# Kernel optimization log

Hardware: AMD Instinct MI355X
Metric: run time of the kernel (lower is better)

The kernel has to match this reference:

```python
import jax, jax.numpy as jnp
import numpy as np

GRID_RES = 128
K_PATHS = 8
SIGMA = 0.8
OFFSETS = jnp.array([[0,0,0],[0,0,1],[0,1,0],[0,1,1],[1,0,0],[1,0,1],[1,1,0],[1,1,1]], dtype=jnp.int32)


def setup_inputs() -> dict:
    key = jax.random.key(0)
    ks = jax.random.split(key, 8)
    N = 500000
    M = 500000
    x_source_ref = jax.random.uniform(ks[0], (N, 3), jnp.float32)
    x_source_curr = jnp.clip(x_source_ref + 0.02 * jax.random.normal(ks[1], (N, 3), jnp.float32), 0.0, 1.0)
    x_query_ref = jax.random.uniform(ks[2], (M, 3), jnp.float32)
    def dense(k, fan_in, fan_out):
        return (jax.random.normal(k, (fan_in, fan_out), jnp.float32) / np.sqrt(fan_in)).astype(jnp.float32)
    return {
        'x_query_ref': x_query_ref,
        'x_source_ref': x_source_ref,
        'x_source_curr': x_source_curr,
        'W_f': dense(ks[3], 3, 3), 'b_f': jnp.zeros((3,), jnp.float32),
        'W_d1': dense(ks[4], 24, 64), 'b_d1': jnp.zeros((64,), jnp.float32),
        'W_d2': dense(ks[5], 64, 64), 'b_d2': jnp.zeros((64,), jnp.float32),
        'W_d3': dense(ks[6], 64, 3), 'b_d3': jnp.zeros((3,), jnp.float32),
    }


def _p2g(content, coords):
    # 8-corner trilinear scatter-add: content [N,C] at float coords [N,3] -> flat grid [R^3, C]
    R = GRID_RES
    base = jnp.floor(coords).astype(jnp.int32)            # [N,3]
    d = coords - base.astype(coords.dtype)                # [N,3] fractional part
    off = OFFSETS[:, None, :]                             # [8,1,3]
    w = jnp.prod(jnp.where(off == 1, d[None], 1.0 - d[None]), axis=-1)  # [8,N]
    idx = base[None] + off                                # [8,N,3]
    flat = (idx[..., 0] * R + idx[..., 1]) * R + idx[..., 2]            # [8,N]
    C = content.shape[-1]
    vals = content[None] * w[..., None]                   # [8,N,C]
    return jnp.zeros((R ** 3, C), content.dtype).at[flat.reshape(-1)].add(vals.reshape(-1, C))


def _trilerp(flat_grid, pts):
    # order-1 map_coordinates, mode='nearest': weights from unclipped coords, indices clipped
    R = GRID_RES
    lo = jnp.floor(pts).astype(jnp.int32)                 # [P,3]
    fr = pts - lo.astype(pts.dtype)
    i0 = jnp.clip(lo, 0, R - 1)
    i1 = jnp.clip(lo + 1, 0, R - 1)
    out = jnp.zeros((pts.shape[0], flat_grid.shape[-1]), flat_grid.dtype)
    for c in range(8):  # fixed 8 corners, keeps peak memory at one [P,C] gather at a time
        ox, oy, oz = OFFSETS[c, 0], OFFSETS[c, 1], OFFSETS[c, 2]
        ix = jnp.where(ox == 1, i1[:, 0], i0[:, 0])
        iy = jnp.where(oy == 1, i1[:, 1], i0[:, 1])
        iz = jnp.where(oz == 1, i1[:, 2], i0[:, 2])
        wx = jnp.where(ox == 1, fr[:, 0], 1.0 - fr[:, 0])
        wy = jnp.where(oy == 1, fr[:, 1], 1.0 - fr[:, 1])
        wz = jnp.where(oz == 1, fr[:, 2], 1.0 - fr[:, 2])
        flat = (ix * R + iy) * R + iz
        out = out + flat_grid[flat] * (wx * wy * wz)[:, None]
    return out


def _posenc(x, L=3):
    outs = []
    for i in range(L):
        freq = (2.0 ** i) * jnp.pi
        outs.append(jnp.sin(freq * x))
        outs.append(jnp.cos(freq * x))
    return jnp.concatenate(outs, axis=-1)


def _forward(x_query_ref, x_source_ref, x_source_curr, W_f, b_f, W_d1, b_d1, W_d2, b_d2, W_d3, b_d3):
    R = GRID_RES
    xs = jnp.clip(x_source_ref, 0.0, 1.0)
    xq = jnp.clip(x_query_ref, 0.0, 1.0)
    u = x_source_curr - xs
    f_trans = jax.nn.gelu(u @ W_f + b_f)
    content = jnp.concatenate([f_trans, jnp.ones((u.shape[0], 1), u.dtype), u], axis=-1)  # [N,7]
    coords = jnp.clip(xs * (R - 1), 0.0, R - 1.001)
    flat_grid = _p2g(content, coords)                     # [R^3, 7]
    q = xq * (R - 1)                                      # [M,3]
    M = q.shape[0]
    noise = jax.random.normal(jax.random.key(42), (K_PATHS, M, 3), q.dtype) * SIGMA
    pts = (q[None] + noise).reshape(-1, 3)                # [K*M,3]
    samples = _trilerp(flat_grid, pts).reshape(K_PATHS, M, -1)
    raw = jnp.mean(samples, axis=0)                       # [M,7]
    grid_f, grid_d, grid_u = raw[:, :3], raw[:, 3:4], raw[:, 4:7]
    denom = jnp.maximum(grid_d, 1e-5)
    mask = (grid_d > 1e-5).astype(raw.dtype)
    f_norm = grid_f / denom * mask
    u_norm = grid_u / denom * mask
    dec = jnp.concatenate([f_norm, u_norm, _posenc(xq)], axis=-1)  # [M,24]
    h = jax.nn.gelu(dec @ W_d1 + b_d1)
    h = jax.nn.gelu(h @ W_d2 + b_d2)
    res = h @ W_d3 + b_d3
    return jnp.clip(u_norm + res, 0.001, 0.999)


def reference(x_query_ref, x_source_ref, x_source_curr, W_f, b_f, W_d1, b_d1, W_d2, b_d2, W_d3, b_d3):
    return _forward(x_query_ref, x_source_ref, x_source_curr, W_f, b_f, W_d1, b_d1, W_d2, b_d2, W_d3, b_d3)
```

## Files before the change

kernel.cpp:

```cpp
#include <hip/hip_runtime.h>
#include <cstdint>

#ifndef JAX_PARTITIONABLE
#define JAX_PARTITIONABLE 1
#endif

#define NCELLS (128*128*128)
#define SCAN_BLOCKS 1024
#define NQBINS (32*32*32)

typedef _Float16 f16;
typedef f16  half8 __attribute__((ext_vector_type(8)));
typedef f16  half4 __attribute__((ext_vector_type(4)));
typedef float f32x4 __attribute__((ext_vector_type(4)));

#define WSTR 40
#define DSTR 40
#define W2STR 72

#define GRID_SCALE 1024.0f
#define GRID_ISCALE 0.0009765625f

__device__ __forceinline__ uint32_t rotl32(uint32_t v, int s){ return (v << s) | (v >> (32 - s)); }

__device__ __forceinline__ void tf2x32(uint32_t& x0, uint32_t& x1){
  const uint32_t k0 = 0u, k1 = 42u;
  const uint32_t k2 = 0x1BD11BDAu ^ k0 ^ k1;
  x0 += k0; x1 += k1;
#define TFR(r) { x0 += x1; x1 = rotl32(x1,(r)); x1 ^= x0; }
  TFR(13) TFR(15) TFR(26) TFR(6)
  x0 += k1; x1 += k2 + 1u;
  TFR(17) TFR(29) TFR(16) TFR(24)
  x0 += k2; x1 += k0 + 2u;
  TFR(13) TFR(15) TFR(26) TFR(6)
  x0 += k0; x1 += k1 + 3u;
  TFR(17) TFR(29) TFR(16) TFR(24)
  x0 += k1; x1 += k2 + 4u;
  TFR(13) TFR(15) TFR(26) TFR(6)
  x0 += k2; x1 += k0 + 5u;
#undef TFR
}

__device__ __forceinline__ float erfinv_xla(float x){
  float w = -log1pf(-x*x);
  float p;
  if (w < 5.0f){
    w -= 2.5f;
    p =  2.81022636e-08f;
    p = fmaf(p,w, 3.43273939e-07f);
    p = fmaf(p,w,-3.5233877e-06f);
    p = fmaf(p,w,-4.39150654e-06f);
    p = fmaf(p,w, 0.00021858087f);
    p = fmaf(p,w,-0.00125372503f);
    p = fmaf(p,w,-0.00417768164f);
    p = fmaf(p,w, 0.246640727f);
    p = fmaf(p,w, 1.50140941f);
  } else {
    w = sqrtf(w) - 3.0f;
    p = -0.000200214257f;
    p = fmaf(p,w, 0.000100950558f);
    p = fmaf(p,w, 0.00134934322f);
    p = fmaf(p,w,-0.00367342844f);
    p = fmaf(p,w, 0.00573950773f);
    p = fmaf(p,w,-0.0076224613f);
    p = fmaf(p,w, 0.00943887047f);
    p = fmaf(p,w, 1.00167406f);
    p = fmaf(p,w, 2.83297682f);
  }
  return p*x;
}

__device__ __forceinline__ float noise_at(uint32_t idx, uint32_t half){
#if JAX_PARTITIONABLE
  (void)half;
  uint32_t x0 = 0u, x1 = idx;
  tf2x32(x0, x1);
  uint32_t bits = x0 ^ x1;
#else
  uint32_t j  = (idx < half) ? idx : (idx - half);
  uint32_t x0 = j, x1 = j + half;
  tf2x32(x0, x1);
  uint32_t bits = (idx < half) ? x0 : x1;
#endif
  float f = __uint_as_float((bits >> 9) | 0x3f800000u) - 1.0f;
  float u = fmaxf(-0.99999994f, fmaf(f, 2.0f, -0.99999994f));
  return (1.41421356f * erfinv_xla(u)) * 0.8f;
}

__device__ __forceinline__ float gelu_f(float x){
  float t = x*x;
  float inner = x * fmaf(0.035677408136f, t, 0.7978845608028654f);
  float e = __expf(2.0f * inner);
  float r = __builtin_amdgcn_rcpf(e + 1.0f);
  return x - x*r;
}

__device__ __forceinline__ uint32_t pack2h(float a, float b){
  union { f16 h[2]; uint32_t u; } c;
  c.h[0] = (f16)(a * GRID_SCALE);
  c.h[1] = (f16)(b * GRID_SCALE);
  return c.u;
}

__device__ __forceinline__ void particle_cell(const float* xsr, int i,
                                              float& sx, float& sy, float& sz,
                                              int& bx, int& by, int& bz,
                                              float& dx, float& dy, float& dz){
  sx = fminf(fmaxf(xsr[3*i+0], 0.0f), 1.0f);
  sy = fminf(fmaxf(xsr[3*i+1], 0.0f), 1.0f);
  sz = fminf(fmaxf(xsr[3*i+2], 0.0f), 1.0f);
  float cx = fminf(fmaxf(sx*127.0f, 0.0f), 126.999f);
  float cy = fminf(fmaxf(sy*127.0f, 0.0f), 126.999f);
  float cz = fminf(fmaxf(sz*127.0f, 0.0f), 126.999f);
  float bxf = floorf(cx), byf = floorf(cy), bzf = floorf(cz);
  bx = (int)bxf; by = (int)byf; bz = (int)bzf;
  dx = cx - bxf; dy = cy - byf; dz = cz - bzf;
}

__device__ __forceinline__ int qbin_of(float qx01, float qy01, float qz01){
  int bx = min((int)(qx01*127.0f), 127) >> 2;
  int by = min((int)(qy01*127.0f), 127) >> 2;
  int bz = min((int)(qz01*127.0f), 127) >> 2;
  return (((bx<<5)+by)<<5)+bz;
}

__global__ void __launch_bounds__(256) hist2_kernel(
    const float* __restrict__ xsr, const float* __restrict__ xq,
    int* __restrict__ cnt, int* __restrict__ qcnt, int N, int M){
  int i = blockIdx.x*256 + threadIdx.x;
  if (i < N){
    float sx,sy,sz,dx,dy,dz; int bx,by,bz;
    particle_cell(xsr,i,sx,sy,sz,bx,by,bz,dx,dy,dz);
    atomicAdd(&cnt[(((bx<<7)+by)<<7)+bz], 1);
  }
  if (i < M){
    float qx01 = fminf(fmaxf(xq[3*i+0], 0.0f), 1.0f);
    float qy01 = fminf(fmaxf(xq[3*i+1], 0.0f), 1.0f);
    float qz01 = fminf(fmaxf(xq[3*i+2], 0.0f), 1.0f);
    atomicAdd(&qcnt[qbin_of(qx01,qy01,qz01)], 1);
  }
}

__global__ void __launch_bounds__(256) scan1_kernel(const int* __restrict__ cnt,
                                                    int* __restrict__ offs,
                                                    int* __restrict__ bsum){
  __shared__ int lds[256];
  int t = threadIdx.x;
  int base = blockIdx.x*2048 + t*8;
  const int4* c4 = reinterpret_cast<const int4*>(cnt + base);
  int4 a0 = c4[0], a1 = c4[1];
  int s = a0.x+a0.y+a0.z+a0.w + a1.x+a1.y+a1.z+a1.w;
  lds[t] = s; __syncthreads();
  for (int off = 1; off < 256; off <<= 1){
    int v = (t >= off) ? lds[t-off] : 0;
    __syncthreads();
    lds[t] += v;
    __syncthreads();
  }
  int run = lds[t] - s;
  if (t == 255) bsum[blockIdx.x] = lds[255];
  int* o = offs + base;
  o[0]=run; run+=a0.x; o[1]=run; run+=a0.y; o[2]=run; run+=a0.z; o[3]=run; run+=a0.w;
  o[4]=run; run+=a1.x; o[5]=run; run+=a1.y; o[6]=run; run+=a1.z; o[7]=run;
}

__global__ void __launch_bounds__(1024) scan2q_kernel(int* __restrict__ bsum,
                                                      const int* __restrict__ qcnt,
                                                      int* __restrict__ qcur){
  __shared__ int lds[1024];
  int t = threadIdx.x;
  int v = bsum[t];
  lds[t] = v; __syncthreads();
  for (int off = 1; off < 1024; off <<= 1){
    int u = (t >= off) ? lds[t-off] : 0;
    __syncthreads();
    lds[t] += u;
    __syncthreads();
  }
  bsum[t] = lds[t] - v;
  if (t == 1023) bsum[1024] = lds[1023];
  __syncthreads();
  int base = t*32;
  int loc[32];
  int s = 0;
#pragma unroll
  for (int j = 0; j < 32; ++j){ loc[j] = qcnt[base+j]; s += loc[j]; }
  lds[t] = s; __syncthreads();
  for (int off = 1; off < 1024; off <<= 1){
    int u = (t >= off) ? lds[t-off] : 0;
    __syncthreads();
    lds[t] += u;
    __syncthreads();
  }
  int run = lds[t] - s;
#pragma unroll
  for (int j = 0; j < 32; ++j){ qcur[base+j] = run; run += loc[j]; }
}

__global__ void __launch_bounds__(256) scan3_kernel(int* __restrict__ offs,
                                                    const int* __restrict__ bsum,
                                                    int* __restrict__ cursor){
  int i = blockIdx.x*256 + threadIdx.x;
  int o = offs[i] + bsum[i >> 11];
  offs[i] = o; cursor[i] = o;
  if (i == 0) offs[NCELLS] = bsum[SCAN_BLOCKS];
}

__global__ void __launch_bounds__(256) scatter2_kernel(
    const float* __restrict__ xsr, const float* __restrict__ xsc,
    const float* __restrict__ Wf,  const float* __restrict__ bf,
    const float* __restrict__ xq,
    int* __restrict__ cursor, int* __restrict__ qcur,
    float4* __restrict__ pf, float4* __restrict__ pu, float* __restrict__ pz,
    float* __restrict__ qs, int* __restrict__ qidx, int N, int M){
  int i = blockIdx.x*256 + threadIdx.x;
  if (i < N){
    float sx,sy,sz,dx,dy,dz; int bx,by,bz;
    particle_cell(xsr,i,sx,sy,sz,bx,by,bz,dx,dy,dz);
    float ux = xsc[3*i+0] - sx;
    float uy = xsc[3*i+1] - sy;
    float uz = xsc[3*i+2] - sz;
    float f0 = gelu_f(ux*Wf[0] + uy*Wf[3] + uz*Wf[6] + bf[0]);
    float f1 = gelu_f(ux*Wf[1] + uy*Wf[4] + uz*Wf[7] + bf[1]);
    float f2 = gelu_f(ux*Wf[2] + uy*Wf[5] + uz*Wf[8] + bf[2]);
    int bin = (((bx<<7)+by)<<7)+bz;
    int pos = atomicAdd(&cursor[bin], 1);
    pf[pos] = make_float4(f0, f1, f2, dx);
    pu[pos] = make_float4(ux, uy, uz, dy);
    pz[pos] = dz;
  }
  if (i < M){
    float qx01 = fminf(fmaxf(xq[3*i+0], 0.0f), 1.0f);
    float qy01 = fminf(fmaxf(xq[3*i+1], 0.0f), 1.0f);
    float qz01 = fminf(fmaxf(xq[3*i+2], 0.0f), 1.0f);
    int pos = atomicAdd(&qcur[qbin_of(qx01,qy01,qz01)], 1);
    qs[3*pos+0] = qx01; qs[3*pos+1] = qy01; qs[3*pos+2] = qz01;
    qidx[pos] = i;
  }
}

__global__ void __launch_bounds__(256) p2g_gather_pair_kernel(
    const int* __restrict__ offs,
    const float4* __restrict__ pf, const float4* __restrict__ pu,
    const float* __restrict__ pz, uint4* __restrict__ gridh){
  int tid = blockIdx.x*256 + threadIdx.x;
  int zg = tid & 63, y = (tid >> 6) & 127, x = tid >> 13;
  int z0 = zg << 1;
  float a0[2]={0,0},a1[2]={0,0},a2[2]={0,0},a3[2]={0,0},a4[2]={0,0},a5[2]={0,0},a6[2]={0,0};
#pragma unroll
  for (int ox = 0; ox < 2; ++ox){
    int bx = x - ox; if (bx < 0) continue;
#pragma unroll
    for (int oy = 0; oy < 2; ++oy){
      int by = y - oy; if (by < 0) continue;
      int b0 = ((((bx<<7)+by)<<7)) + z0;
      int em = offs[b0];
      int sm = (z0 > 0) ? offs[b0-1] : em;
      int e0 = offs[b0+1];
      int e1 = offs[b0+2];
      for (int p = sm; p < e1; ++p){
        float4 A = pf[p]; float4 B = pu[p]; float dz = pz[p];
        float wx = ox ? A.w : 1.0f - A.w;
        float wy = oy ? B.w : 1.0f - B.w;
        float wxy = wx*wy;
        float omdz = 1.0f - dz;
        float w0 = (p < em) ? dz : ((p < e0) ? omdz : 0.0f);
        float w1 = (p < em) ? 0.0f : ((p < e0) ? dz : omdz);
        w0 *= wxy; w1 *= wxy;
        a0[0]=fmaf(A.x,w0,a0[0]); a1[0]=fmaf(A.y,w0,a1[0]); a2[0]=fmaf(A.z,w0,a2[0]);
        a3[0]+=w0; a4[0]=fmaf(B.x,w0,a4[0]); a5[0]=fmaf(B.y,w0,a5[0]); a6[0]=fmaf(B.z,w0,a6[0]);
        a0[1]=fmaf(A.x,w1,a0[1]); a1[1]=fmaf(A.y,w1,a1[1]); a2[1]=fmaf(A.z,w1,a2[1]);
        a3[1]+=w1; a4[1]=fmaf(B.x,w1,a4[1]); a5[1]=fmaf(B.y,w1,a5[1]); a6[1]=fmaf(B.z,w1,a6[1]);
      }
    }
  }
  int cell0 = ((((x<<7)+y)<<7)) + z0;
  uint4 g0, g1;
  g0.x = pack2h(a0[0], a1[0]); g0.y = pack2h(a2[0], a4[0]);
  g0.z = pack2h(a5[0], a6[0]); g0.w = __float_as_uint(a3[0]);
  g1.x = pack2h(a0[1], a1[1]); g1.y = pack2h(a2[1], a4[1]);
  g1.z = pack2h(a5[1], a6[1]); g1.w = __float_as_uint(a3[1]);
  uint4* g = gridh + cell0;
  g[0] = g0; g[1] = g1;
}

__global__ void __launch_bounds__(256, 4) gather_mlp_sorted_kernel(
    const float* __restrict__ qs,  const int* __restrict__ qidx,
    const uint4* __restrict__ gridh,
    const float* __restrict__ W1,  const float* __restrict__ b1,
    const float* __restrict__ W2,  const float* __restrict__ b2,
    const float* __restrict__ W3,  const float* __restrict__ b3,
    float* __restrict__ out, int M, int nblk)
{
  __shared__ __align__(16) f16  decs[4][64*DSTR];
  __shared__ __align__(16) f16  w1t[64*WSTR];
  __shared__ __align__(16) f16  w2t[64*W2STR];
  __shared__ __align__(16) float b1s[64], b2s[64];
  __shared__ __align__(16) float w3s[64*4];

  for (int i = threadIdx.x; i < 64*32; i += 256){
    int n = i >> 5, k = i & 31;
    w1t[n*WSTR + k] = (k < 24) ? (f16)W1[k*64 + n] : (f16)0.0f;
  }
  for (int i = threadIdx.x; i < 64*64; i += 256){
    int n = i >> 6, k = i & 63;
    w2t[n*W2STR + k] = (f16)W2[k*64 + n];
  }
  if (threadIdx.x < 64){ b1s[threadIdx.x] = b1[threadIdx.x]; b2s[threadIdx.x] = b2[threadIdx.x]; }
  for (int i = threadIdx.x; i < 192; i += 256){
    w3s[(i/3)*4 + (i - (i/3)*3)] = W3[i];
  }
  __syncthreads();

  int b = blockIdx.x;
  int nb8 = (nblk >> 3) << 3;
  int c = (b < nb8) ? ((b & 7)*(nblk >> 3) + (b >> 3)) : b;
  int t = c*256 + (int)threadIdx.x;
  bool active = (t < M);
  int tc = active ? t : (M - 1);
  int m = qidx[tc];

  float qx01 = qs[3*tc+0], qy01 = qs[3*tc+1], qz01 = qs[3*tc+2];
  float qx = qx01*127.0f, qy = qy01*127.0f, qz = qz01*127.0f;

  float r0=0.f,r1=0.f,r2=0.f,r3=0.f,r4=0.f,r5=0.f,r6=0.f;
  const uint32_t KSTRIDE = 3u*(uint32_t)M;
  const uint32_t HALF    = 4u*KSTRIDE;
  uint32_t m3 = 3u*(uint32_t)m;

  for (int k = 0; k < 8; ++k) {
    uint32_t base = (uint32_t)k*KSTRIDE + m3;
    float px = qx + noise_at(base+0u, HALF);
    float py = qy + noise_at(base+1u, HALF);
    float pz = qz + noise_at(base+2u, HALF);
    float fxf = floorf(px), fyf = floorf(py), fzf = floorf(pz);
    float fx = px - fxf, fy = py - fyf, fz = pz - fzf;
    int lx = (int)fxf, ly = (int)fyf, lz = (int)fzf;
    int x0i = min(max(lx,0),127),   x1i = min(max(lx+1,0),127);
    int y0i = min(max(ly,0),127),   y1i = min(max(ly+1,0),127);
    int z0i = min(max(lz,0),127),   z1i = min(max(lz+1,0),127);
    float ex = 1.0f-fx, ey = 1.0f-fy, ez = 1.0f-fz;

    auto corner = [&](int xi,int yi,int zi,float w){
      uint4 q4 = gridh[(((xi<<7)+yi)<<7)+zi];
      union { uint32_t u; f16 h[2]; } c0, c1, c2;
      c0.u = q4.x; c1.u = q4.y; c2.u = q4.z;
      r0 = fmaf((float)c0.h[0], w, r0);
      r1 = fmaf((float)c0.h[1], w, r1);
      r2 = fmaf((float)c1.h[0], w, r2);
      r4 = fmaf((float)c1.h[1], w, r4);
      r5 = fmaf((float)c2.h[0], w, r5);
      r6 = fmaf((float)c2.h[1], w, r6);
      r3 = fmaf(__uint_as_float(q4.w), w, r3);
    };
    corner(x0i,y0i,z0i, ex*ey*ez);
    corner(x0i,y0i,z1i, ex*ey*fz);
    corner(x0i,y1i,z0i, ex*fy*ez);
    corner(x0i,y1i,z1i, ex*fy*fz);
    corner(x1i,y0i,z0i, fx*ey*ez);
    corner(x1i,y0i,z1i, fx*ey*fz);
    corner(x1i,y1i,z0i, fx*fy*ez);
    corner(x1i,y1i,z1i, fx*fy*fz);
  }

  float dmean = r3*0.125f;
  float denom = fmaxf(dmean, 1e-5f);
  float maskf = (dmean > 1e-5f) ? 1.0f : 0.0f;
  float s   = 0.125f/denom*maskf;
  float sfu = s * GRID_ISCALE;
  float un0 = r4*sfu, un1 = r5*sfu, un2 = r6*sfu;

  float dec[24];
  dec[0]=r0*sfu; dec[1]=r1*sfu; dec[2]=r2*sfu; dec[3]=un0; dec[4]=un1; dec[5]=un2;
  dec[6]  = __builtin_amdgcn_sinf(0.5f*qx01);
  dec[7]  = __builtin_amdgcn_sinf(0.5f*qy01);
  dec[8]  = __builtin_amdgcn_sinf(0.5f*qz01);
  dec[9]  = __builtin_amdgcn_cosf(0.5f*qx01);
  dec[10] = __builtin_amdgcn_cosf(0.5f*qy01);
  dec[11] = __builtin_amdgcn_cosf(0.5f*qz01);
  dec[12] = __builtin_amdgcn_sinf(qx01);
  dec[13] = __builtin_amdgcn_sinf(qy01);
  dec[14] = __builtin_amdgcn_sinf(qz01);
  dec[15] = __builtin_amdgcn_cosf(qx01);
  dec[16] = __builtin_amdgcn_cosf(qy01);
  dec[17] = __builtin_amdgcn_cosf(qz01);
  dec[18] = __builtin_amdgcn_sinf(2.0f*qx01);
  dec[19] = __builtin_amdgcn_sinf(2.0f*qy01);
  dec[20] = __builtin_amdgcn_sinf(2.0f*qz01);
  dec[21] = __builtin_amdgcn_cosf(2.0f*qx01);
  dec[22] = __builtin_amdgcn_cosf(2.0f*qy01);
  dec[23] = __builtin_amdgcn_cosf(2.0f*qz01);

  int lane = threadIdx.x & 63;
  int wv   = threadIdx.x >> 6;
  f16* hb = &decs[wv][0];
  int lo = lane & 15;
  int hi = lane >> 4;

  {
    half8 dh;
#pragma unroll
    for (int c4 = 0; c4 < 3; ++c4){
#pragma unroll
      for (int j = 0; j < 8; ++j) dh[j] = (f16)dec[c4*8 + j];
      *reinterpret_cast<half8*>(&hb[lane*DSTR + c4*8]) = dh;
    }
#pragma unroll
    for (int j = 0; j < 8; ++j) dh[j] = (f16)0.0f;
    *reinterpret_cast<half8*>(&hb[lane*DSTR + 24]) = dh;
  }

  half4 w1f[4][2];
#pragma unroll
  for (int a = 0; a < 4; ++a)
#pragma unroll
    for (int kb = 0; kb < 2; ++kb)
      w1f[a][kb] = *reinterpret_cast<const half4*>(&w1t[(16*a + lo)*WSTR + 16*kb + 4*hi]);

  half4 dff[4][2];
#pragma unroll
  for (int bq = 0; bq < 4; ++bq)
#pragma unroll
    for (int kb = 0; kb < 2; ++kb)
      dff[bq][kb] = *reinterpret_cast<const half4*>(&hb[(16*bq + lo)*DSTR + 16*kb + 4*hi]);

  half4 hv[4][4];
#pragma unroll
  for (int a = 0; a < 4; ++a){
    f32x4 zb = *reinterpret_cast<const f32x4*>(&b1s[16*a + 4*hi]);
#pragma unroll
    for (int bq = 0; bq < 4; ++bq){
      f32x4 z = __builtin_amdgcn_mfma_f32_16x16x16f16(w1f[a][0], dff[bq][0], zb, 0, 0, 0);
      z       = __builtin_amdgcn_mfma_f32_16x16x16f16(w1f[a][1], dff[bq][1], z,  0, 0, 0);
      half4 hvv;
#pragma unroll
      for (int p = 0; p < 4; ++p) hvv[p] = (f16)gelu_f(z[p]);
      hv[a][bq] = hvv;
    }
  }

  float part[4][3];
#pragma unroll
  for (int bq = 0; bq < 4; ++bq){ part[bq][0]=0.f; part[bq][1]=0.f; part[bq][2]=0.f; }

#pragma unroll
  for (int a2 = 0; a2 < 4; ++a2){
    half4 w2f[4];
#pragma unroll
    for (int kb = 0; kb < 4; ++kb)
      w2f[kb] = *reinterpret_cast<const half4*>(&w2t[(16*a2 + lo)*W2STR + 16*kb + 4*hi]);
    f32x4 zb2 = *reinterpret_cast<const f32x4*>(&b2s[16*a2 + 4*hi]);
#pragma unroll
    for (int bq = 0; bq < 4; ++bq){
      f32x4 z = __builtin_amdgcn_mfma_f32_16x16x16f16(w2f[0], hv[0][bq], zb2, 0, 0, 0);
      z       = __builtin_amdgcn_mfma_f32_16x16x16f16(w2f[1], hv[1][bq], z,   0, 0, 0);
      z       = __builtin_amdgcn_mfma_f32_16x16x16f16(w2f[2], hv[2][bq], z,   0, 0, 0);
      z       = __builtin_amdgcn_mfma_f32_16x16x16f16(w2f[3], hv[3][bq], z,   0, 0, 0);
#pragma unroll
      for (int p = 0; p < 4; ++p){
        f32x4 w3v = *reinterpret_cast<const f32x4*>(&w3s[(16*a2 + 4*hi + p)*4]);
        float g = gelu_f(z[p]);
        part[bq][0] = fmaf(g, w3v[0], part[bq][0]);
        part[bq][1] = fmaf(g, w3v[1], part[bq][1]);
        part[bq][2] = fmaf(g, w3v[2], part[bq][2]);
      }
    }
  }

#pragma unroll
  for (int bq = 0; bq < 4; ++bq)
#pragma unroll
    for (int cc = 0; cc < 3; ++cc){
      float v = part[bq][cc];
      v += __shfl_xor(v, 16, 64);
      v += __shfl_xor(v, 32, 64);
      part[bq][cc] = v;
    }

  float o0 = (hi==0) ? part[0][0] : (hi==1) ? part[1][0] : (hi==2) ? part[2][0] : part[3][0];
  float o1 = (hi==0) ? part[0][1] : (hi==1) ? part[1][1] : (hi==2) ? part[2][1] : part[3][1];
  float o2 = (hi==0) ? part[0][2] : (hi==1) ? part[1][2] : (hi==2) ? part[2][2] : part[3][2];
  o0 += b3[0]; o1 += b3[1]; o2 += b3[2];

  if (active){
    out[3*m+0] = fminf(fmaxf(un0 + o0, 0.001f), 0.999f);
    out[3*m+1] = fminf(fmaxf(un1 + o1, 0.001f), 0.999f);
    out[3*m+2] = fminf(fmaxf(un2 + o2, 0.001f), 0.999f);
  }
}

__global__ void __launch_bounds__(256) p2g_atomic_kernel(
    const float* __restrict__ xsr, const float* __restrict__ xsc,
    const float* __restrict__ Wf,  const float* __restrict__ bf,
    float* __restrict__ grid, int N)
{
  int i = blockIdx.x*256 + threadIdx.x;
  if (i >= N) return;
  float sx,sy,sz,dx,dy,dz; int bx,by,bz;
  particle_cell(xsr,i,sx,sy,sz,bx,by,bz,dx,dy,dz);
  float ux = xsc[3*i+0] - sx;
  float uy = xsc[3*i+1] - sy;
  float uz = xsc[3*i+2] - sz;
  float f0 = gelu_f(ux*Wf[0] + uy*Wf[3] + uz*Wf[6] + bf[0]);
  float f1 = gelu_f(ux*Wf[1] + uy*Wf[4] + uz*Wf[7] + bf[1]);
  float f2 = gelu_f(ux*Wf[2] + uy*Wf[5] + uz*Wf[8] + bf[2]);
  float ex = 1.0f - dx, ey = 1.0f - dy, ez = 1.0f - dz;
  auto splat = [&](int xi, int yi, int zi, float w){
    float* p = grid + ((size_t)((((xi<<7)+yi)<<7)+zi) << 3);
    unsafeAtomicAdd(p+0, f0*w);
    unsafeAtomicAdd(p+1, f1*w);
    unsafeAtomicAdd(p+2, f2*w);
    unsafeAtomicAdd(p+3, w);
    unsafeAtomicAdd(p+4, ux*w);
    unsafeAtomicAdd(p+5, uy*w);
    unsafeAtomicAdd(p+6, uz*w);
  };
  splat(bx,  by,  bz,   ex*ey*ez);
  splat(bx,  by,  bz+1, ex*ey*dz);
  splat(bx,  by+1,bz,   ex*dy*ez);
  splat(bx,  by+1,bz+1, ex*dy*dz);
  splat(bx+1,by,  bz,   dx*ey*ez);
  splat(bx+1,by,  bz+1, dx*ey*dz);
  splat(bx+1,by+1,bz,   dx*dy*ez);
  splat(bx+1,by+1,bz+1, dx*dy*dz);
}

__global__ void __launch_bounds__(256) grid2half_kernel(
    const float* __restrict__ grid, uint4* __restrict__ gridh){
  int i = blockIdx.x*256 + threadIdx.x;
  const float4* p = reinterpret_cast<const float4*>(grid + ((size_t)i << 3));
  float4 A = p[0], B = p[1];
  uint4 g;
  g.x = pack2h(A.x, A.y);
  g.y = pack2h(A.z, B.x);
  g.z = pack2h(B.y, B.z);
  g.w = __float_as_uint(A.w);
  gridh[i] = g;
}

__global__ void __launch_bounds__(256) qident_kernel(
    const float* __restrict__ xq, float* __restrict__ qs, int* __restrict__ qidx, int M){
  int i = blockIdx.x*256 + threadIdx.x;
  if (i >= M) return;
  qs[3*i+0] = fminf(fmaxf(xq[3*i+0], 0.0f), 1.0f);
  qs[3*i+1] = fminf(fmaxf(xq[3*i+1], 0.0f), 1.0f);
  qs[3*i+2] = fminf(fmaxf(xq[3*i+2], 0.0f), 1.0f);
  qidx[i] = i;
}

extern "C" void kernel_launch(void* const* d_in, const int* in_sizes, int n_in,
                              void* d_out, int out_size, void* d_ws, size_t ws_size,
                              hipStream_t stream)
{
  const float* xq  = (const float*)d_in[0];
  const float* xsr = (const float*)d_in[1];
  const float* xsc = (const float*)d_in[2];
  const float* Wf  = (const float*)d_in[3];
  const float* bf  = (const float*)d_in[4];
  const float* W1  = (const float*)d_in[5];
  const float* b1  = (const float*)d_in[6];
  const float* W2  = (const float*)d_in[7];
  const float* b2  = (const float*)d_in[8];
  const float* W3  = (const float*)d_in[9];
  const float* b3  = (const float*)d_in[10];
  float* out  = (float*)d_out;
  int M = in_sizes[0]/3;
  int N = in_sizes[1]/3;

  char* W = (char*)d_ws;
  size_t off = 0;
  auto alloc = [&](size_t bytes){ size_t o = off; off = (off + bytes + 255) & ~(size_t)255; return o; };
  size_t o_grid   = alloc((size_t)NCELLS * 8 * sizeof(float));
  size_t o_cnt    = alloc((size_t)NCELLS * sizeof(int));
  size_t o_qcnt   = alloc((size_t)NQBINS * sizeof(int));
  size_t o_offs   = alloc(((size_t)NCELLS + 1) * sizeof(int));
  size_t o_cursor = alloc((size_t)NCELLS * sizeof(int));
  size_t o_bsum   = alloc((size_t)(SCAN_BLOCKS + 1) * sizeof(int));
  size_t o_qcur   = alloc((size_t)NQBINS * sizeof(int));
  size_t o_pf     = alloc((size_t)N * sizeof(float4));
  size_t o_pu     = alloc((size_t)N * sizeof(float4));
  size_t o_pz     = alloc((size_t)N * sizeof(float));
  size_t o_qs     = alloc((size_t)M * 3 * sizeof(float));
  size_t o_qidx   = alloc((size_t)M * sizeof(int));
  size_t full_end = off;

  float*  grid   = (float*)(W + o_grid);
  int*    cnt    = (int*)(W + o_cnt);
  int*    qcnt   = (int*)(W + o_qcnt);
  int*    offs   = (int*)(W + o_offs);
  int*    cursor = (int*)(W + o_cursor);
  int*    bsum   = (int*)(W + o_bsum);
  int*    qcur   = (int*)(W + o_qcur);
  float4* pf     = (float4*)(W + o_pf);
  float4* pu     = (float4*)(W + o_pu);
  float*  pz     = (float*)(W + o_pz);
  float*  qs     = (float*)(W + o_qs);
  int*    qidx   = (int*)(W + o_qidx);

  int nthr = (N > M) ? N : M;
  int nblkNM = (nthr + 255) / 256;
  uint4* gridh;

  if (full_end <= ws_size) {
    gridh = (uint4*)(W + o_grid);
    hipMemsetAsync(cnt, 0, (size_t)NCELLS * sizeof(int) + (size_t)NQBINS * sizeof(int), stream);
    hist2_kernel<<<nblkNM, 256, 0, stream>>>(xsr, xq, cnt, qcnt, N, M);
    scan1_kernel<<<SCAN_BLOCKS, 256, 0, stream>>>(cnt, offs, bsum);
    scan2q_kernel<<<1, 1024, 0, stream>>>(bsum, qcnt, qcur);
    scan3_kernel<<<NCELLS/256, 256, 0, stream>>>(offs, bsum, cursor);
    scatter2_kernel<<<nblkNM, 256, 0, stream>>>(xsr, xsc, Wf, bf, xq, cursor, qcur,
                                                pf, pu, pz, qs, qidx, N, M);
    p2g_gather_pair_kernel<<<(NCELLS/2)/256, 256, 0, stream>>>(offs, pf, pu, pz, gridh);
  } else {
    gridh = (uint4*)(W + o_offs);
    hipMemsetAsync(grid, 0, (size_t)NCELLS * 8 * sizeof(float), stream);
    p2g_atomic_kernel<<<(N+255)/256, 256, 0, stream>>>(xsr, xsc, Wf, bf, grid, N);
    grid2half_kernel<<<NCELLS/256, 256, 0, stream>>>(grid, gridh);
    qident_kernel<<<(M+255)/256, 256, 0, stream>>>(xq, qs, qidx, M);
  }

  int nblk = (M + 255) / 256;
  gather_mlp_sorted_kernel<<<nblk, 256, 0, stream>>>(qs, qidx, gridh, W1,b1,W2,b2,W3,b3, out, M, nblk);
}
```

Before: 352.6 us.

## Replace counting-sort P2G with direct packed-half atomic splatting into grid

Removes the cell histogram, three-stage prefix scan, particle scatter, and gather-based P2G. Each particle now splats its 8 trilinear corner contributions straight into the final 16-byte packed grid with half2 atomics for the scaled features and an fp32 atomic for the weight. The query histogram, scan and scatter move into their own small kernels. This drops several launches and the intermediate particle buffers, but relies on packed fp16 atomic adds whose contention and rounding during accumulation differ from the old fp32 sums. That may hurt accuracy.

```diff
diff --git a/kernel.cpp b/kernel.cpp
--- a/kernel.cpp
+++ b/kernel.cpp
@@ -1,4 +1,5 @@
 #include <hip/hip_runtime.h>
+#include <hip/hip_fp16.h>
 #include <cstdint>
 
 #ifndef JAX_PARTITIONABLE
@@ -6,7 +7,6 @@
 #endif
 
 #define NCELLS (128*128*128)
-#define SCAN_BLOCKS 1024
 #define NQBINS (32*32*32)
 
 typedef _Float16 f16;
@@ -95,13 +95,6 @@
   return x - x*r;
 }
 
-__device__ __forceinline__ uint32_t pack2h(float a, float b){
-  union { f16 h[2]; uint32_t u; } c;
-  c.h[0] = (f16)(a * GRID_SCALE);
-  c.h[1] = (f16)(b * GRID_SCALE);
-  return c.u;
-}
-
 __device__ __forceinline__ void particle_cell(const float* xsr, int i,
                                               float& sx, float& sy, float& sz,
                                               int& bx, int& by, int& bz,
@@ -124,14 +117,42 @@
   return (((bx<<5)+by)<<5)+bz;
 }
 
-__global__ void __launch_bounds__(256) hist2_kernel(
-    const float* __restrict__ xsr, const float* __restrict__ xq,
-    int* __restrict__ cnt, int* __restrict__ qcnt, int N, int M){
+__global__ void __launch_bounds__(256) p2gq_atomic_kernel(
+    const float* __restrict__ xsr, const float* __restrict__ xsc,
+    const float* __restrict__ Wf,  const float* __restrict__ bf,
+    const float* __restrict__ xq,
+    uint32_t* __restrict__ gridh, int* __restrict__ qcnt, int N, int M)
+{
   int i = blockIdx.x*256 + threadIdx.x;
   if (i < N){
     float sx,sy,sz,dx,dy,dz; int bx,by,bz;
     particle_cell(xsr,i,sx,sy,sz,bx,by,bz,dx,dy,dz);
-    atomicAdd(&cnt[(((bx<<7)+by)<<7)+bz], 1);
+    float ux = xsc[3*i+0] - sx;
+    float uy = xsc[3*i+1] - sy;
+    float uz = xsc[3*i+2] - sz;
+    float F0 = gelu_f(ux*Wf[0] + uy*Wf[3] + uz*Wf[6] + bf[0]) * GRID_SCALE;
+    float F1 = gelu_f(ux*Wf[1] + uy*Wf[4] + uz*Wf[7] + bf[1]) * GRID_SCALE;
+    float F2 = gelu_f(ux*Wf[2] + uy*Wf[5] + uz*Wf[8] + bf[2]) * GRID_SCALE;
+    float U0 = ux * GRID_SCALE, U1 = uy * GRID_SCALE, U2 = uz * GRID_SCALE;
+    float ex = 1.0f - dx, ey = 1.0f - dy, ez = 1.0f - dz;
+    auto splat = [&](int xi, int yi, int zi, float w){
+      uint32_t* p = gridh + ((size_t)((((xi<<7)+yi)<<7)+zi) << 2);
+      unsafeAtomicAdd(reinterpret_cast<__half2*>(p+0),
+                      __halves2half2(__float2half(F0*w), __float2half(F1*w)));
+      unsafeAtomicAdd(reinterpret_cast<__half2*>(p+1),
+                      __halves2half2(__float2half(F2*w), __float2half(U0*w)));
+      unsafeAtomicAdd(reinterpret_cast<__half2*>(p+2),
+                      __halves2half2(__float2half(U1*w), __float2half(U2*w)));
+      unsafeAtomicAdd(reinterpret_cast<float*>(p+3), w);
+    };
+    splat(bx,  by,  bz,   ex*ey*ez);
+    splat(bx,  by,  bz+1, ex*ey*dz);
+    splat(bx,  by+1,bz,   ex*dy*ez);
+    splat(bx,  by+1,bz+1, ex*dy*dz);
+    splat(bx+1,by,  bz,   dx*ey*ez);
+    splat(bx+1,by,  bz+1, dx*ey*dz);
+    splat(bx+1,by+1,bz,   dx*dy*ez);
+    splat(bx+1,by+1,bz+1, dx*dy*dz);
   }
   if (i < M){
     float qx01 = fminf(fmaxf(xq[3*i+0], 0.0f), 1.0f);
@@ -141,45 +162,10 @@
   }
 }
 
-__global__ void __launch_bounds__(256) scan1_kernel(const int* __restrict__ cnt,
-                                                    int* __restrict__ offs,
-                                                    int* __restrict__ bsum){
-  __shared__ int lds[256];
-  int t = threadIdx.x;
-  int base = blockIdx.x*2048 + t*8;
-  const int4* c4 = reinterpret_cast<const int4*>(cnt + base);
-  int4 a0 = c4[0], a1 = c4[1];
-  int s = a0.x+a0.y+a0.z+a0.w + a1.x+a1.y+a1.z+a1.w;
-  lds[t] = s; __syncthreads();
-  for (int off = 1; off < 256; off <<= 1){
-    int v = (t >= off) ? lds[t-off] : 0;
-    __syncthreads();
-    lds[t] += v;
-    __syncthreads();
-  }
-  int run = lds[t] - s;
-  if (t == 255) bsum[blockIdx.x] = lds[255];
-  int* o = offs + base;
-  o[0]=run; run+=a0.x; o[1]=run; run+=a0.y; o[2]=run; run+=a0.z; o[3]=run; run+=a0.w;
-  o[4]=run; run+=a1.x; o[5]=run; run+=a1.y; o[6]=run; run+=a1.z; o[7]=run;
-}
-
-__global__ void __launch_bounds__(1024) scan2q_kernel(int* __restrict__ bsum,
-                                                      const int* __restrict__ qcnt,
-                                                      int* __restrict__ qcur){
+__global__ void __launch_bounds__(1024) qscan_kernel(const int* __restrict__ qcnt,
+                                                     int* __restrict__ qcur){
   __shared__ int lds[1024];
   int t = threadIdx.x;
-  int v = bsum[t];
-  lds[t] = v; __syncthreads();
-  for (int off = 1; off < 1024; off <<= 1){
-    int u = (t >= off) ? lds[t-off] : 0;
-    __syncthreads();
-    lds[t] += u;
-    __syncthreads();
-  }
-  bsum[t] = lds[t] - v;
-  if (t == 1023) bsum[1024] = lds[1023];
-  __syncthreads();
   int base = t*32;
   int loc[32];
   int s = 0;
@@ -197,91 +183,17 @@
   for (int j = 0; j < 32; ++j){ qcur[base+j] = run; run += loc[j]; }
 }
 
-__global__ void __launch_bounds__(256) scan3_kernel(int* __restrict__ offs,
-                                                    const int* __restrict__ bsum,
-                                                    int* __restrict__ cursor){
+__global__ void __launch_bounds__(256) scatterq_kernel(
+    const float* __restrict__ xq, int* __restrict__ qcur,
+    float* __restrict__ qs, int* __restrict__ qidx, int M){
   int i = blockIdx.x*256 + threadIdx.x;
-  int o = offs[i] + bsum[i >> 11];
-  offs[i] = o; cursor[i] = o;
-  if (i == 0) offs[NCELLS] = bsum[SCAN_BLOCKS];
-}
-
-__global__ void __launch_bounds__(256) scatter2_kernel(
-    const float* __restrict__ xsr, const float* __restrict__ xsc,
-    const float* __restrict__ Wf,  const float* __restrict__ bf,
-    const float* __restrict__ xq,
-    int* __restrict__ cursor, int* __restrict__ qcur,
-    float4* __restrict__ pf, float4* __restrict__ pu, float* __restrict__ pz,
-    float* __restrict__ qs, int* __restrict__ qidx, int N, int M){
-  int i = blockIdx.x*256 + threadIdx.x;
-  if (i < N){
-    float sx,sy,sz,dx,dy,dz; int bx,by,bz;
-    particle_cell(xsr,i,sx,sy,sz,bx,by,bz,dx,dy,dz);
-    float ux = xsc[3*i+0] - sx;
-    float uy = xsc[3*i+1] - sy;
-    float uz = xsc[3*i+2] - sz;
-    float f0 = gelu_f(ux*Wf[0] + uy*Wf[3] + uz*Wf[6] + bf[0]);
-    float f1 = gelu_f(ux*Wf[1] + uy*Wf[4] + uz*Wf[7] + bf[1]);
-    float f2 = gelu_f(ux*Wf[2] + uy*Wf[5] + uz*Wf[8] + bf[2]);
-    int bin = (((bx<<7)+by)<<7)+bz;
-    int pos = atomicAdd(&cursor[bin], 1);
-    pf[pos] = make_float4(f0, f1, f2, dx);
-    pu[pos] = make_float4(ux, uy, uz, dy);
-    pz[pos] = dz;
-  }
-  if (i < M){
-    float qx01 = fminf(fmaxf(xq[3*i+0], 0.0f), 1.0f);
-    float qy01 = fminf(fmaxf(xq[3*i+1], 0.0f), 1.0f);
-    float qz01 = fminf(fmaxf(xq[3*i+2], 0.0f), 1.0f);
-    int pos = atomicAdd(&qcur[qbin_of(qx01,qy01,qz01)], 1);
-    qs[3*pos+0] = qx01; qs[3*pos+1] = qy01; qs[3*pos+2] = qz01;
-    qidx[pos] = i;
-  }
-}
-
-__global__ void __launch_bounds__(256) p2g_gather_pair_kernel(
-    const int* __restrict__ offs,
-    const float4* __restrict__ pf, const float4* __restrict__ pu,
-    const float* __restrict__ pz, uint4* __restrict__ gridh){
-  int tid = blockIdx.x*256 + threadIdx.x;
-  int zg = tid & 63, y = (tid >> 6) & 127, x = tid >> 13;
-  int z0 = zg << 1;
-  float a0[2]={0,0},a1[2]={0,0},a2[2]={0,0},a3[2]={0,0},a4[2]={0,0},a5[2]={0,0},a6[2]={0,0};
-#pragma unroll
-  for (int ox = 0; ox < 2; ++ox){
-    int bx = x - ox; if (bx < 0) continue;
-#pragma unroll
-    for (int oy = 0; oy < 2; ++oy){
-      int by = y - oy; if (by < 0) continue;
-      int b0 = ((((bx<<7)+by)<<7)) + z0;
-      int em = offs[b0];
-      int sm = (z0 > 0) ? offs[b0-1] : em;
-      int e0 = offs[b0+1];
-      int e1 = offs[b0+2];
-      for (int p = sm; p < e1; ++p){
-        float4 A = pf[p]; float4 B = pu[p]; float dz = pz[p];
-        float wx = ox ? A.w : 1.0f - A.w;
-        float wy = oy ? B.w : 1.0f - B.w;
-        float wxy = wx*wy;
-        float omdz = 1.0f - dz;
-        float w0 = (p < em) ? dz : ((p < e0) ? omdz : 0.0f);
-        float w1 = (p < em) ? 0.0f : ((p < e0) ? dz : omdz);
-        w0 *= wxy; w1 *= wxy;
-        a0[0]=fmaf(A.x,w0,a0[0]); a1[0]=fmaf(A.y,w0,a1[0]); a2[0]=fmaf(A.z,w0,a2[0]);
-        a3[0]+=w0; a4[0]=fmaf(B.x,w0,a4[0]); a5[0]=fmaf(B.y,w0,a5[0]); a6[0]=fmaf(B.z,w0,a6[0]);
-        a0[1]=fmaf(A.x,w1,a0[1]); a1[1]=fmaf(A.y,w1,a1[1]); a2[1]=fmaf(A.z,w1,a2[1]);
-        a3[1]+=w1; a4[1]=fmaf(B.x,w1,a4[1]); a5[1]=fmaf(B.y,w1,a5[1]); a6[1]=fmaf(B.z,w1,a6[1]);
-      }
-    }
-  }
-  int cell0 = ((((x<<7)+y)<<7)) + z0;
-  uint4 g0, g1;
-  g0.x = pack2h(a0[0], a1[0]); g0.y = pack2h(a2[0], a4[0]);
-  g0.z = pack2h(a5[0], a6[0]); g0.w = __float_as_uint(a3[0]);
-  g1.x = pack2h(a0[1], a1[1]); g1.y = pack2h(a2[1], a4[1]);
-  g1.z = pack2h(a5[1], a6[1]); g1.w = __float_as_uint(a3[1]);
-  uint4* g = gridh + cell0;
-  g[0] = g0; g[1] = g1;
+  if (i >= M) return;
+  float qx01 = fminf(fmaxf(xq[3*i+0], 0.0f), 1.0f);
+  float qy01 = fminf(fmaxf(xq[3*i+1], 0.0f), 1.0f);
+  float qz01 = fminf(fmaxf(xq[3*i+2], 0.0f), 1.0f);
+  int pos = atomicAdd(&qcur[qbin_of(qx01,qy01,qz01)], 1);
+  qs[3*pos+0] = qx01; qs[3*pos+1] = qy01; qs[3*pos+2] = qz01;
+  qidx[pos] = i;
 }
 
 __global__ void __launch_bounds__(256, 4) gather_mlp_sorted_kernel(
@@ -489,65 +401,6 @@
   }
 }
 
-__global__ void __launch_bounds__(256) p2g_atomic_kernel(
-    const float* __restrict__ xsr, const float* __restrict__ xsc,
-    const float* __restrict__ Wf,  const float* __restrict__ bf,
-    float* __restrict__ grid, int N)
-{
-  int i = blockIdx.x*256 + threadIdx.x;
-  if (i >= N) return;
-  float sx,sy,sz,dx,dy,dz; int bx,by,bz;
-  particle_cell(xsr,i,sx,sy,sz,bx,by,bz,dx,dy,dz);
-  float ux = xsc[3*i+0] - sx;
-  float uy = xsc[3*i+1] - sy;
-  float uz = xsc[3*i+2] - sz;
-  float f0 = gelu_f(ux*Wf[0] + uy*Wf[3] + uz*Wf[6] + bf[0]);
-  float f1 = gelu_f(ux*Wf[1] + uy*Wf[4] + uz*Wf[7] + bf[1]);
-  float f2 = gelu_f(ux*Wf[2] + uy*Wf[5] + uz*Wf[8] + bf[2]);
-  float ex = 1.0f - dx, ey = 1.0f - dy, ez = 1.0f - dz;
-  auto splat = [&](int xi, int yi, int zi, float w){
-    float* p = grid + ((size_t)((((xi<<7)+yi)<<7)+zi) << 3);
-    unsafeAtomicAdd(p+0, f0*w);
-    unsafeAtomicAdd(p+1, f1*w);
-    unsafeAtomicAdd(p+2, f2*w);
-    unsafeAtomicAdd(p+3, w);
-    unsafeAtomicAdd(p+4, ux*w);
-    unsafeAtomicAdd(p+5, uy*w);
-    unsafeAtomicAdd(p+6, uz*w);
-  };
-  splat(bx,  by,  bz,   ex*ey*ez);
-  splat(bx,  by,  bz+1, ex*ey*dz);
-  splat(bx,  by+1,bz,   ex*dy*ez);
-  splat(bx,  by+1,bz+1, ex*dy*dz);
-  splat(bx+1,by,  bz,   dx*ey*ez);
-  splat(bx+1,by,  bz+1, dx*ey*dz);
-  splat(bx+1,by+1,bz,   dx*dy*ez);
-  splat(bx+1,by+1,bz+1, dx*dy*dz);
-}
-
-__global__ void __launch_bounds__(256) grid2half_kernel(
-    const float* __restrict__ grid, uint4* __restrict__ gridh){
-  int i = blockIdx.x*256 + threadIdx.x;
-  const float4* p = reinterpret_cast<const float4*>(grid + ((size_t)i << 3));
-  float4 A = p[0], B = p[1];
-  uint4 g;
-  g.x = pack2h(A.x, A.y);
-  g.y = pack2h(A.z, B.x);
-  g.z = pack2h(B.y, B.z);
-  g.w = __float_as_uint(A.w);
-  gridh[i] = g;
-}
-
-__global__ void __launch_bounds__(256) qident_kernel(
-    const float* __restrict__ xq, float* __restrict__ qs, int* __restrict__ qidx, int M){
-  int i = blockIdx.x*256 + threadIdx.x;
-  if (i >= M) return;
-  qs[3*i+0] = fminf(fmaxf(xq[3*i+0], 0.0f), 1.0f);
-  qs[3*i+1] = fminf(fmaxf(xq[3*i+1], 0.0f), 1.0f);
-  qs[3*i+2] = fminf(fmaxf(xq[3*i+2], 0.0f), 1.0f);
-  qidx[i] = i;
-}
-
 extern "C" void kernel_launch(void* const* d_in, const int* in_sizes, int n_in,
                               void* d_out, int out_size, void* d_ws, size_t ws_size,
                               hipStream_t stream)
@@ -570,55 +423,28 @@
   char* W = (char*)d_ws;
   size_t off = 0;
   auto alloc = [&](size_t bytes){ size_t o = off; off = (off + bytes + 255) & ~(size_t)255; return o; };
-  size_t o_grid   = alloc((size_t)NCELLS * 8 * sizeof(float));
-  size_t o_cnt    = alloc((size_t)NCELLS * sizeof(int));
-  size_t o_qcnt   = alloc((size_t)NQBINS * sizeof(int));
-  size_t o_offs   = alloc(((size_t)NCELLS + 1) * sizeof(int));
-  size_t o_cursor = alloc((size_t)NCELLS * sizeof(int));
-  size_t o_bsum   = alloc((size_t)(SCAN_BLOCKS + 1) * sizeof(int));
-  size_t o_qcur   = alloc((size_t)NQBINS * sizeof(int));
-  size_t o_pf     = alloc((size_t)N * sizeof(float4));
-  size_t o_pu     = alloc((size_t)N * sizeof(float4));
-  size_t o_pz     = alloc((size_t)N * sizeof(float));
-  size_t o_qs     = alloc((size_t)M * 3 * sizeof(float));
-  size_t o_qidx   = alloc((size_t)M * sizeof(int));
-  size_t full_end = off;
-
-  float*  grid   = (float*)(W + o_grid);
-  int*    cnt    = (int*)(W + o_cnt);
-  int*    qcnt   = (int*)(W + o_qcnt);
-  int*    offs   = (int*)(W + o_offs);
-  int*    cursor = (int*)(W + o_cursor);
-  int*    bsum   = (int*)(W + o_bsum);
-  int*    qcur   = (int*)(W + o_qcur);
-  float4* pf     = (float4*)(W + o_pf);
-  float4* pu     = (float4*)(W + o_pu);
-  float*  pz     = (float*)(W + o_pz);
-  float*  qs     = (float*)(W + o_qs);
-  int*    qidx   = (int*)(W + o_qidx);
+  size_t o_gridh = alloc((size_t)NCELLS * 16);
+  size_t o_qcnt  = alloc((size_t)NQBINS * sizeof(int));
+  size_t o_qcur  = alloc((size_t)NQBINS * sizeof(int));
+  size_t o_qs    = alloc((size_t)M * 3 * sizeof(float));
+  size_t o_qidx  = alloc((size_t)M * sizeof(int));
+  (void)ws_size;
+
+  uint32_t* gridh = (uint32_t*)(W + o_gridh);
+  int*      qcnt  = (int*)(W + o_qcnt);
+  int*      qcur  = (int*)(W + o_qcur);
+  float*    qs    = (float*)(W + o_qs);
+  int*      qidx  = (int*)(W + o_qidx);
 
   int nthr = (N > M) ? N : M;
   int nblkNM = (nthr + 255) / 256;
-  uint4* gridh;
-
-  if (full_end <= ws_size) {
-    gridh = (uint4*)(W + o_grid);
-    hipMemsetAsync(cnt, 0, (size_t)NCELLS * sizeof(int) + (size_t)NQBINS * sizeof(int), stream);
-    hist2_kernel<<<nblkNM, 256, 0, stream>>>(xsr, xq, cnt, qcnt, N, M);
-    scan1_kernel<<<SCAN_BLOCKS, 256, 0, stream>>>(cnt, offs, bsum);
-    scan2q_kernel<<<1, 1024, 0, stream>>>(bsum, qcnt, qcur);
-    scan3_kernel<<<NCELLS/256, 256, 0, stream>>>(offs, bsum, cursor);
-    scatter2_kernel<<<nblkNM, 256, 0, stream>>>(xsr, xsc, Wf, bf, xq, cursor, qcur,
-                                                pf, pu, pz, qs, qidx, N, M);
-    p2g_gather_pair_kernel<<<(NCELLS/2)/256, 256, 0, stream>>>(offs, pf, pu, pz, gridh);
-  } else {
-    gridh = (uint4*)(W + o_offs);
-    hipMemsetAsync(grid, 0, (size_t)NCELLS * 8 * sizeof(float), stream);
-    p2g_atomic_kernel<<<(N+255)/256, 256, 0, stream>>>(xsr, xsc, Wf, bf, grid, N);
-    grid2half_kernel<<<NCELLS/256, 256, 0, stream>>>(grid, gridh);
-    qident_kernel<<<(M+255)/256, 256, 0, stream>>>(xq, qs, qidx, M);
-  }
+
+  hipMemsetAsync(gridh, 0, (size_t)NCELLS * 16 + (size_t)NQBINS * sizeof(int), stream);
+  p2gq_atomic_kernel<<<nblkNM, 256, 0, stream>>>(xsr, xsc, Wf, bf, xq, gridh, qcnt, N, M);
+  qscan_kernel<<<1, 1024, 0, stream>>>(qcnt, qcur);
+  scatterq_kernel<<<(M+255)/256, 256, 0, stream>>>(xq, qcur, qs, qidx, M);
 
   int nblk = (M + 255) / 256;
-  gather_mlp_sorted_kernel<<<nblk, 256, 0, stream>>>(qs, qidx, gridh, W1,b1,W2,b2,W3,b3, out, M, nblk);
-}
+  gather_mlp_sorted_kernel<<<nblk, 256, 0, stream>>>(qs, qidx, (const uint4*)gridh,
+                                                     W1,b1,W2,b2,W3,b3, out, M, nblk);
+}
```

Result: slower. 1.071 ms (+203.8%).
